# Kernel tuning notes

Measured on AMD Instinct MI355X. Metric: run time of the kernel, lower is better.

The kernel has to match this reference:

```python
import jax, jax.numpy as jnp
import numpy as np

NN = 50000   # num nodes
NE = 10000   # num hyperedges
E = 300000   # num incidences
H = 256      # h_dim == input_dim


def _prelu(x, alpha):
    return jnp.where(x > 0, x, alpha * x)


def setup_inputs() -> dict:
    key = jax.random.key(0)
    ks = jax.random.split(key, 16)
    s = 1.0 / np.sqrt(H)
    inp = {
        "n_feat": jax.random.normal(ks[0], (NN, H), jnp.float32),
        "he_feat": jax.random.normal(ks[1], (NE, H), jnp.float32),
        "node_idx": jax.random.randint(ks[2], (E,), 0, NN),
        "hedge_idx": jax.random.randint(ks[3], (E,), 0, NE),
        # positive degree-style normalization tensors (offset avoids div-by-~0)
        "node_reg_weight": jax.random.uniform(ks[4], (NN,), jnp.float32) + 0.5,
        "node_reg_sum": jax.random.uniform(ks[5], (NN,), jnp.float32) + 0.5,
        "hedge_reg_weight": jax.random.uniform(ks[6], (NE,), jnp.float32) + 0.5,
        "hedge_reg_sum": jax.random.uniform(ks[7], (NE,), jnp.float32) + 0.5,
        # learned params
        "W_in": jax.random.uniform(ks[8], (H, H), jnp.float32, -s, s),
        "b_in": jax.random.uniform(ks[9], (H,), jnp.float32, -s, s),
        "W_n2e": jax.random.uniform(ks[10], (H, H), jnp.float32, -s, s),
        "b_n2e": jax.random.uniform(ks[11], (H,), jnp.float32, -s, s),
        "W_e2n": jax.random.uniform(ks[12], (H, H), jnp.float32, -s, s),
        "b_e2n": jax.random.uniform(ks[13], (H,), jnp.float32, -s, s),
        "alpha": jnp.asarray(0.25, jnp.float32),  # PReLU (single shared param)
    }
    return inp


def reference(n_feat, he_feat, node_idx, hedge_idx,
              node_reg_weight, node_reg_sum, hedge_reg_weight, hedge_reg_sum,
              W_in, b_in, W_n2e, b_n2e, W_e2n, b_e2n, alpha):
    # input2hidden
    nfeat = n_feat @ W_in.T + b_in                       # [NN, H]

    # --- node -> hedge ('in' edges: src=node, dst=hedge) ---
    Wh_n = nfeat @ W_n2e.T + b_n2e                       # [NN, H]
    w_in = node_reg_weight[node_idx] / hedge_reg_sum[hedge_idx]   # [E]
    msg = w_in[:, None] * Wh_n[node_idx]                 # [E, H] gather-multiply
    h_hedge = jax.ops.segment_sum(msg, hedge_idx, num_segments=NE)
    efeat = _prelu(h_hedge, alpha)                       # [NE, H]

    # --- hedge -> node ('con' edges: src=hedge, dst=node) ---
    Wh_e = efeat @ W_e2n.T + b_e2n                       # [NE, H]
    w_con = hedge_reg_weight[hedge_idx] / node_reg_sum[node_idx]  # [E]
    msg2 = w_con[:, None] * Wh_e[hedge_idx]              # [E, H]
    h_node = jax.ops.segment_sum(msg2, node_idx, num_segments=NN)
    nfeat_out = _prelu(h_node, alpha)                    # [NN, H]

    return nfeat_out, efeat
```

## Files before the change

### kernel.cpp

```cpp
#include <hip/hip_runtime.h>

#define NNODE  50000
#define NHEDGE 10000
#define NEDGE  300000
#define HD     256
#define NS     (NHEDGE + NNODE)
#define CVT32_B (((NNODE*HD)/32 + 255) / 256)
#define PAD    32
#define CAP_H  128
#define CAP_N  48

typedef __attribute__((ext_vector_type(8))) short bf16x8;
typedef __attribute__((ext_vector_type(8))) unsigned short u16x8;
typedef __attribute__((ext_vector_type(4))) float f32x4;

__device__ __forceinline__ float prelu(float v, float a){ return v > 0.f ? v : a*v; }
__device__ __forceinline__ unsigned short f2bf(float f){
  unsigned u = __float_as_uint(f);
  return (unsigned short)((u + 0x7FFFu + ((u>>16)&1u)) >> 16);
}
__device__ __forceinline__ float bf2f(unsigned short h){
  return __uint_as_float(((unsigned)h) << 16);
}
__device__ __forceinline__ unsigned f2fp8(float x){
  unsigned u = __float_as_uint(x * 0x1p-120f);
  unsigned s = (u >> 24) & 0x80u;
  unsigned m = u & 0x7fffffffu;
  unsigned r = m + 0x7ffffu + ((m >> 20) & 1u);
  unsigned v = r >> 20;
  if(v > 0x7eu) v = 0x7eu;
  return v | s;
}
__device__ __forceinline__ float fp82f(unsigned b){
  unsigned mag = (b & 0x7fu) << 20;
  float f = __uint_as_float(mag) * 0x1p120f;
  return __uint_as_float(__float_as_uint(f) | ((b & 0x80u) << 24));
}

__global__ __launch_bounds__(256) void k_prep0(
    const float* __restrict__ W_in, const float* __restrict__ b_in,
    const float* __restrict__ W_n2e, const float* __restrict__ b_n2e,
    const float* __restrict__ W_e2n, const float* __restrict__ n_feat,
    const float* __restrict__ nrw,
    unsigned short* __restrict__ Wb0, unsigned short* __restrict__ Wb1,
    float* __restrict__ bc, int* __restrict__ cnts,
    unsigned char* __restrict__ tab8){
  int blk = blockIdx.x, t = threadIdx.x;
  if(blk < HD){
    int o = blk;
    int zi = o*256 + t;
    if(zi < NS) cnts[(size_t)zi*PAD] = 0;
    __shared__ float wn[HD];
    __shared__ float red[4];
    wn[t] = W_n2e[(size_t)o*HD + t];
    __syncthreads();
    float pb = wn[t] * b_in[t];
    #pragma unroll
    for(int d = 32; d > 0; d >>= 1) pb += __shfl_down(pb, d);
    if((t & 63) == 0) red[t >> 6] = pb;
    float acc = 0.f;
    #pragma unroll 8
    for(int h = 0; h < HD; ++h) acc += wn[h] * W_in[(size_t)h*HD + t];
    Wb0[(size_t)o*HD + t] = f2bf(acc);
    Wb1[(size_t)o*HD + t] = f2bf(W_e2n[(size_t)o*HD + t]);
    __syncthreads();
    if(t == 0) bc[o] = red[0] + red[1] + red[2] + red[3] + b_n2e[o];
  } else {
    int t32 = (blk - HD)*256 + t;
    if(t32 >= (NNODE*HD)/32) return;
    size_t f = (size_t)t32 * 32;
    float w = nrw[f >> 8];
    const float4* f4 = (const float4*)(n_feat + f);
    unsigned q[8];
    #pragma unroll
    for(int g = 0; g < 8; ++g){
      float4 a = f4[g];
      q[g] =  f2fp8(w*a.x)        | (f2fp8(w*a.y) << 8)
           | (f2fp8(w*a.z) << 16) | (f2fp8(w*a.w) << 24);
    }
    uint4* out = (uint4*)(tab8 + f);
    out[0] = make_uint4(q[0], q[1], q[2], q[3]);
    out[1] = make_uint4(q[4], q[5], q[6], q[7]);
  }
}

__global__ void k_histfill(const int* __restrict__ node_idx, const int* __restrict__ hedge_idx,
                           const float* __restrict__ nrw, int* __restrict__ cnts,
                           int2* __restrict__ bkt_h, int* __restrict__ bkt_n){
  int e = blockIdx.x*256 + threadIdx.x;
  if(e < NEDGE){
    int j = hedge_idx[e];
    int n = node_idx[e];
    int p = atomicAdd(&cnts[(size_t)j*PAD], 1);
    if(p < CAP_H) bkt_h[(size_t)j*CAP_H + p] = make_int2(n, __float_as_int(nrw[n]));
    int q = atomicAdd(&cnts[(size_t)(NHEDGE + n)*PAD], 1);
    if(q < CAP_N) bkt_n[(size_t)n*CAP_N + q] = j;
  }
}

#define A1_STAGE(V,W) \
    { uint2 cv = V; float cw = W; \
      if(k + 8 < cnt){ int2 s = bh[k+8]; W = __int_as_float(s.y); V = tab[(size_t)s.x*32 + sl]; } \
      acc[0] += fp82f(cv.x);       acc[1] += fp82f(cv.x >> 8); \
      acc[2] += fp82f(cv.x >> 16); acc[3] += fp82f(cv.x >> 24); \
      acc[4] += fp82f(cv.y);       acc[5] += fp82f(cv.y >> 8); \
      acc[6] += fp82f(cv.y >> 16); acc[7] += fp82f(cv.y >> 24); \
      sw += cw; } \
    if(++k >= cnt) break;

__global__ __launch_bounds__(256) void k_agg1(const unsigned char* __restrict__ tab8,
        const int2* __restrict__ bkt_h, const int* __restrict__ cnts,
        unsigned short* __restrict__ aggx_b, float* __restrict__ aggw){
  int wv = threadIdx.x >> 6, lane = threadIdx.x & 63;
  int sub = lane >> 5, sl = lane & 31;
  int j = blockIdx.x*8 + wv*2 + sub;
  int cnt = cnts[(size_t)j*PAD]; if(cnt > CAP_H) cnt = CAP_H;
  const int2* bh = bkt_h + (size_t)j*CAP_H;
  const uint2* tab = (const uint2*)tab8;
  float acc[8] = {0.f,0.f,0.f,0.f,0.f,0.f,0.f,0.f};
  float sw = 0.f;
  uint2 z2 = make_uint2(0,0);
  uint2 v0=z2,v1=z2,v2=z2,v3=z2,v4=z2,v5=z2,v6=z2,v7=z2;
  float w0=0,w1=0,w2=0,w3=0,w4=0,w5=0,w6=0,w7=0;
  if(cnt > 0){ int2 s = bh[0]; w0 = __int_as_float(s.y); v0 = tab[(size_t)s.x*32 + sl]; }
  if(cnt > 1){ int2 s = bh[1]; w1 = __int_as_float(s.y); v1 = tab[(size_t)s.x*32 + sl]; }
  if(cnt > 2){ int2 s = bh[2]; w2 = __int_as_float(s.y); v2 = tab[(size_t)s.x*32 + sl]; }
  if(cnt > 3){ int2 s = bh[3]; w3 = __int_as_float(s.y); v3 = tab[(size_t)s.x*32 + sl]; }
  if(cnt > 4){ int2 s = bh[4]; w4 = __int_as_float(s.y); v4 = tab[(size_t)s.x*32 + sl]; }
  if(cnt > 5){ int2 s = bh[5]; w5 = __int_as_float(s.y); v5 = tab[(size_t)s.x*32 + sl]; }
  if(cnt > 6){ int2 s = bh[6]; w6 = __int_as_float(s.y); v6 = tab[(size_t)s.x*32 + sl]; }
  if(cnt > 7){ int2 s = bh[7]; w7 = __int_as_float(s.y); v7 = tab[(size_t)s.x*32 + sl]; }
  int k = 0;
  while(k < cnt){
    A1_STAGE(v0, w0)
    A1_STAGE(v1, w1)
    A1_STAGE(v2, w2)
    A1_STAGE(v3, w3)
    A1_STAGE(v4, w4)
    A1_STAGE(v5, w5)
    A1_STAGE(v6, w6)
    A1_STAGE(v7, w7)
  }
  u16x8 ob;
  #pragma unroll
  for(int c = 0; c < 8; ++c) ob[c] = f2bf(acc[c]);
  ((u16x8*)aggx_b)[(size_t)j*32 + sl] = ob;
  if(sl == 0) aggw[j] = sw;
}

__global__ __launch_bounds__(256) void k_gemm01(
    const unsigned short* __restrict__ xb, const unsigned short* __restrict__ Wb0,
    const unsigned short* __restrict__ Wb1,
    const float* __restrict__ aggw, const float* __restrict__ hrs,
    const float* __restrict__ hrw, const float* __restrict__ bc,
    const float* __restrict__ be, const float* __restrict__ alpha_p,
    float* __restrict__ out_ef, unsigned short* __restrict__ ef_b,
    unsigned short* __restrict__ y_b){
  int wv = threadIdx.x >> 6, lane = threadIdx.x & 63;
  int m0 = blockIdx.x*32;
  int n0 = wv*64;
  int lr = lane & 15, lk = (lane >> 4) << 3, rb = (lane >> 4) << 2;
  float alpha = *alpha_p;
  const bf16x8 zero8 = {0,0,0,0,0,0,0,0};
  {
    f32x4 acc[2][4];
    #pragma unroll
    for(int a = 0; a < 2; ++a)
      #pragma unroll
      for(int b = 0; b < 4; ++b) acc[a][b] = (f32x4){0.f,0.f,0.f,0.f};
    #pragma unroll
    for(int kc = 0; kc < HD; kc += 32){
      bf16x8 af[2], bfr[4];
      #pragma unroll
      for(int mi = 0; mi < 2; ++mi){
        int r = m0 + mi*16 + lr;
        af[mi] = (r < NHEDGE) ? *(const bf16x8*)&xb[(size_t)r*HD + kc + lk] : zero8;
      }
      #pragma unroll
      for(int ni = 0; ni < 4; ++ni){
        int c = n0 + ni*16 + lr;
        bfr[ni] = *(const bf16x8*)&Wb0[(size_t)c*HD + kc + lk];
      }
      #pragma unroll
      for(int mi = 0; mi < 2; ++mi)
        #pragma unroll
        for(int ni = 0; ni < 4; ++ni)
          acc[mi][ni] = __builtin_amdgcn_mfma_f32_16x16x32_bf16(af[mi], bfr[ni], acc[mi][ni], 0, 0, 0);
    }
    #pragma unroll
    for(int mi = 0; mi < 2; ++mi){
      #pragma unroll
      for(int jj = 0; jj < 4; ++jj){
        int r = m0 + mi*16 + rb + jj;
        if(r < NHEDGE){
          float ra = aggw[r];
          float inv = 1.f / hrs[r];
          #pragma unroll
          for(int ni = 0; ni < 4; ++ni){
            int c = n0 + ni*16 + lr;
            float v = (acc[mi][ni][jj] + ra*bc[c]) * inv;
            v = prelu(v, alpha);
            out_ef[(size_t)r*HD + c] = v;
            ef_b[(size_t)r*HD + c] = f2bf(v);
          }
        }
      }
    }
  }
  __syncthreads();
  {
    f32x4 acc[2][4];
    #pragma unroll
    for(int a = 0; a < 2; ++a)
      #pragma unroll
      for(int b = 0; b < 4; ++b) acc[a][b] = (f32x4){0.f,0.f,0.f,0.f};
    #pragma unroll
    for(int kc = 0; kc < HD; kc += 32){
      bf16x8 af[2], bfr[4];
      #pragma unroll
      for(int mi = 0; mi < 2; ++mi){
        int r = m0 + mi*16 + lr;
        af[mi] = (r < NHEDGE) ? *(const bf16x8*)&ef_b[(size_t)r*HD + kc + lk] : zero8;
      }
      #pragma unroll
      for(int ni = 0; ni < 4; ++ni){
        int c = n0 + ni*16 + lr;
        bfr[ni] = *(const bf16x8*)&Wb1[(size_t)c*HD + kc + lk];
      }
      #pragma unroll
      for(int mi = 0; mi < 2; ++mi)
        #pragma unroll
        for(int ni = 0; ni < 4; ++ni)
          acc[mi][ni] = __builtin_amdgcn_mfma_f32_16x16x32_bf16(af[mi], bfr[ni], acc[mi][ni], 0, 0, 0);
    }
    #pragma unroll
    for(int mi = 0; mi < 2; ++mi){
      #pragma unroll
      for(int jj = 0; jj < 4; ++jj){
        int r = m0 + mi*16 + rb + jj;
        if(r < NHEDGE){
          float ra = hrw[r];
          #pragma unroll
          for(int ni = 0; ni < 4; ++ni){
            int c = n0 + ni*16 + lr;
            float v = ra * (acc[mi][ni][jj] + be[c]);
            y_b[(size_t)r*HD + c] = f2bf(v);
          }
        }
      }
    }
  }
}

__global__ __launch_bounds__(256) void k_agg2(const unsigned short* __restrict__ yb,
        const int* __restrict__ bkt_n, const int* __restrict__ cnts,
        const float* __restrict__ nrs, const float* __restrict__ alpha_p,
        float* __restrict__ out_nodes){
  int wv = threadIdx.x >> 6, lane = threadIdx.x & 63;
  int sub = lane >> 5, sl = lane & 31;
  int i = blockIdx.x*8 + wv*2 + sub;
  int cnt = cnts[(size_t)(NHEDGE + i)*PAD]; if(cnt > CAP_N) cnt = CAP_N;
  const int* bn = bkt_n + (size_t)i*CAP_N;
  const u16x8* tab = (const u16x8*)yb;
  float acc[8] = {0.f,0.f,0.f,0.f,0.f,0.f,0.f,0.f};
  u16x8 z8 = {0,0,0,0,0,0,0,0};
  u16x8 v0=z8, v1=z8, v2=z8, v3=z8;
  if(cnt > 0){ int j = bn[0]; v0 = tab[(size_t)j*32 + sl]; }
  if(cnt > 1){ int j = bn[1]; v1 = tab[(size_t)j*32 + sl]; }
  if(cnt > 2){ int j = bn[2]; v2 = tab[(size_t)j*32 + sl]; }
  if(cnt > 3){ int j = bn[3]; v3 = tab[(size_t)j*32 + sl]; }
  int k = 0;
  while(k < cnt){
    { u16x8 cv = v0;
      if(k + 4 < cnt){ int j = bn[k+4]; v0 = tab[(size_t)j*32 + sl]; }
      #pragma unroll
      for(int c = 0; c < 8; ++c) acc[c] += bf2f(cv[c]); }
    if(++k >= cnt) break;
    { u16x8 cv = v1;
      if(k + 4 < cnt){ int j = bn[k+4]; v1 = tab[(size_t)j*32 + sl]; }
      #pragma unroll
      for(int c = 0; c < 8; ++c) acc[c] += bf2f(cv[c]); }
    if(++k >= cnt) break;
    { u16x8 cv = v2;
      if(k + 4 < cnt){ int j = bn[k+4]; v2 = tab[(size_t)j*32 + sl]; }
      #pragma unroll
      for(int c = 0; c < 8; ++c) acc[c] += bf2f(cv[c]); }
    if(++k >= cnt) break;
    { u16x8 cv = v3;
      if(k + 4 < cnt){ int j = bn[k+4]; v3 = tab[(size_t)j*32 + sl]; }
      #pragma unroll
      for(int c = 0; c < 8; ++c) acc[c] += bf2f(cv[c]); }
    ++k;
  }
  float inv = 1.f / nrs[i];
  float a = *alpha_p;
  float4 o1, o2;
  o1.x = prelu(acc[0]*inv, a); o1.y = prelu(acc[1]*inv, a);
  o1.z = prelu(acc[2]*inv, a); o1.w = prelu(acc[3]*inv, a);
  o2.x = prelu(acc[4]*inv, a); o2.y = prelu(acc[5]*inv, a);
  o2.z = prelu(acc[6]*inv, a); o2.w = prelu(acc[7]*inv, a);
  *(float4*)&out_nodes[(size_t)i*HD + sl*8]     = o1;
  *(float4*)&out_nodes[(size_t)i*HD + sl*8 + 4] = o2;
}

extern "C" void kernel_launch(void* const* d_in, const int* in_sizes, int n_in,
                              void* d_out, int out_size, void* d_ws, size_t ws_size,
                              hipStream_t stream){
  const float* n_feat   = (const float*)d_in[0];
  const int*   node_idx  = (const int*)d_in[2];
  const int*   hedge_idx = (const int*)d_in[3];
  const float* nrw  = (const float*)d_in[4];
  const float* nrs  = (const float*)d_in[5];
  const float* hrw  = (const float*)d_in[6];
  const float* hrs  = (const float*)d_in[7];
  const float* W_in  = (const float*)d_in[8];
  const float* b_in  = (const float*)d_in[9];
  const float* W_n2e = (const float*)d_in[10];
  const float* b_n2e = (const float*)d_in[11];
  const float* W_e2n = (const float*)d_in[12];
  const float* b_e2n = (const float*)d_in[13];
  const float* alpha = (const float*)d_in[14];

  float* out_nodes = (float*)d_out;
  float* out_efeat = out_nodes + (size_t)NNODE * HD;

  unsigned char* tab8 = (unsigned char*)out_nodes;

  char* p = (char*)d_ws;
  auto take = [&](size_t bytes) -> void* {
    void* r = (void*)p;
    p += (bytes + 255) & ~(size_t)255;
    return r;
  };
  unsigned short* Wb0     = (unsigned short*)take((size_t)HD*HD*2);
  unsigned short* Wb1     = (unsigned short*)take((size_t)HD*HD*2);
  float*          bc      = (float*)take(HD*4);
  float*          aggw    = (float*)take(NHEDGE*4);
  unsigned short* aggx_b  = (unsigned short*)take((size_t)NHEDGE*HD*2);
  unsigned short* efeat_b = (unsigned short*)take((size_t)NHEDGE*HD*2);
  int*            cnts    = (int*)take((size_t)NS*PAD*4);
  int2*           bkt_h   = (int2*)take((size_t)NHEDGE*CAP_H*8);
  int*            bkt_n   = (int*)take((size_t)NNODE*CAP_N*4);
  unsigned short* ybuf_b  = aggx_b;

  k_prep0<<<HD + CVT32_B, 256, 0, stream>>>(W_in, b_in, W_n2e, b_n2e, W_e2n,
                                            n_feat, nrw, Wb0, Wb1, bc, cnts, tab8);
  k_histfill<<<(NEDGE+255)/256, 256, 0, stream>>>(node_idx, hedge_idx, nrw,
                                                  cnts, bkt_h, bkt_n);
  k_agg1<<<NHEDGE/8, 256, 0, stream>>>(tab8, bkt_h, cnts, aggx_b, aggw);
  k_gemm01<<<(NHEDGE + 31)/32, 256, 0, stream>>>(aggx_b, Wb0, Wb1, aggw, hrs, hrw,
                                                 bc, b_e2n, alpha,
                                                 out_efeat, efeat_b, ybuf_b);
  k_agg2<<<NNODE/8, 256, 0, stream>>>(ybuf_b, bkt_n, cnts, nrs, alpha, out_nodes);
}
```

Baseline: 150.4 us.

## Split each hyperedge's gather across four half-waves with LDS reduction

k_agg1 now assigns four 32-lane groups to each hyperedge instead of one. Each group takes a quarter of the incidence list, loads its bucket metadata in one coalesced read, broadcasts indices with shuffles, and issues up to 16 independent row gathers before accumulating. The partial sums are then reduced through shared memory. This targets the latency of the serial per-hyperedge gather chain, which averages about 30 incidences, by exposing more parallelism and memory-level concurrency. The cost is four times as many blocks, a __syncthreads, LDS traffic, and more registers for the 16-entry prefetch array.

Result: faster. 133.2 us, median of 2 (-11.4%).

```diff
diff --git a/kernel.cpp b/kernel.cpp
--- a/kernel.cpp
+++ b/kernel.cpp
@@ -98,54 +98,71 @@
   }
 }
 
-#define A1_STAGE(V,W) \
-    { uint2 cv = V; float cw = W; \
-      if(k + 8 < cnt){ int2 s = bh[k+8]; W = __int_as_float(s.y); V = tab[(size_t)s.x*32 + sl]; } \
-      acc[0] += fp82f(cv.x);       acc[1] += fp82f(cv.x >> 8); \
-      acc[2] += fp82f(cv.x >> 16); acc[3] += fp82f(cv.x >> 24); \
-      acc[4] += fp82f(cv.y);       acc[5] += fp82f(cv.y >> 8); \
-      acc[6] += fp82f(cv.y >> 16); acc[7] += fp82f(cv.y >> 24); \
-      sw += cw; } \
-    if(++k >= cnt) break;
-
 __global__ __launch_bounds__(256) void k_agg1(const unsigned char* __restrict__ tab8,
         const int2* __restrict__ bkt_h, const int* __restrict__ cnts,
         unsigned short* __restrict__ aggx_b, float* __restrict__ aggw){
-  int wv = threadIdx.x >> 6, lane = threadIdx.x & 63;
-  int sub = lane >> 5, sl = lane & 31;
-  int j = blockIdx.x*8 + wv*2 + sub;
+  __shared__ float lacc[8][32][9];
+  __shared__ float lsw[8];
+  int tid = threadIdx.x;
+  int half = tid >> 5;
+  int sl   = tid & 31;
+  int lane = tid & 63;
+  int hb   = lane & 32;
+  int j = blockIdx.x*2 + (half >> 2);
+  int c = half & 3;
   int cnt = cnts[(size_t)j*PAD]; if(cnt > CAP_H) cnt = CAP_H;
-  const int2* bh = bkt_h + (size_t)j*CAP_H;
+  int Lc = (cnt + 3) >> 2;
+  int lo = c*Lc; if(lo > cnt) lo = cnt;
+  int hi = lo + Lc; if(hi > cnt) hi = cnt;
+  int Len = hi - lo;
+  const int2* bh = bkt_h + (size_t)j*CAP_H + lo;
+  int2 meta = (sl < Len) ? bh[sl] : make_int2(0, 0);
   const uint2* tab = (const uint2*)tab8;
   float acc[8] = {0.f,0.f,0.f,0.f,0.f,0.f,0.f,0.f};
   float sw = 0.f;
-  uint2 z2 = make_uint2(0,0);
-  uint2 v0=z2,v1=z2,v2=z2,v3=z2,v4=z2,v5=z2,v6=z2,v7=z2;
-  float w0=0,w1=0,w2=0,w3=0,w4=0,w5=0,w6=0,w7=0;
-  if(cnt > 0){ int2 s = bh[0]; w0 = __int_as_float(s.y); v0 = tab[(size_t)s.x*32 + sl]; }
-  if(cnt > 1){ int2 s = bh[1]; w1 = __int_as_float(s.y); v1 = tab[(size_t)s.x*32 + sl]; }
-  if(cnt > 2){ int2 s = bh[2]; w2 = __int_as_float(s.y); v2 = tab[(size_t)s.x*32 + sl]; }
-  if(cnt > 3){ int2 s = bh[3]; w3 = __int_as_float(s.y); v3 = tab[(size_t)s.x*32 + sl]; }
-  if(cnt > 4){ int2 s = bh[4]; w4 = __int_as_float(s.y); v4 = tab[(size_t)s.x*32 + sl]; }
-  if(cnt > 5){ int2 s = bh[5]; w5 = __int_as_float(s.y); v5 = tab[(size_t)s.x*32 + sl]; }
-  if(cnt > 6){ int2 s = bh[6]; w6 = __int_as_float(s.y); v6 = tab[(size_t)s.x*32 + sl]; }
-  if(cnt > 7){ int2 s = bh[7]; w7 = __int_as_float(s.y); v7 = tab[(size_t)s.x*32 + sl]; }
-  int k = 0;
-  while(k < cnt){
-    A1_STAGE(v0, w0)
-    A1_STAGE(v1, w1)
-    A1_STAGE(v2, w2)
-    A1_STAGE(v3, w3)
-    A1_STAGE(v4, w4)
-    A1_STAGE(v5, w5)
-    A1_STAGE(v6, w6)
-    A1_STAGE(v7, w7)
-  }
-  u16x8 ob;
+  uint2 v[16];
   #pragma unroll
-  for(int c = 0; c < 8; ++c) ob[c] = f2bf(acc[c]);
-  ((u16x8*)aggx_b)[(size_t)j*32 + sl] = ob;
-  if(sl == 0) aggw[j] = sw;
+  for(int k = 0; k < 16; ++k){
+    if(k < Len){
+      int src = __shfl(meta.x, hb + k);
+      sw += __int_as_float(__shfl(meta.y, hb + k));
+      v[k] = tab[(size_t)src*32 + sl];
+    }
+  }
+  #pragma unroll
+  for(int k = 0; k < 16; ++k){
+    if(k < Len){
+      uint2 cv = v[k];
+      acc[0] += fp82f(cv.x);       acc[1] += fp82f(cv.x >> 8);
+      acc[2] += fp82f(cv.x >> 16); acc[3] += fp82f(cv.x >> 24);
+      acc[4] += fp82f(cv.y);       acc[5] += fp82f(cv.y >> 8);
+      acc[6] += fp82f(cv.y >> 16); acc[7] += fp82f(cv.y >> 24);
+    }
+  }
+  for(int k = 16; k < Len; ++k){
+    int2 mk = bh[k];
+    sw += __int_as_float(mk.y);
+    uint2 cv = tab[(size_t)mk.x*32 + sl];
+    acc[0] += fp82f(cv.x);       acc[1] += fp82f(cv.x >> 8);
+    acc[2] += fp82f(cv.x >> 16); acc[3] += fp82f(cv.x >> 24);
+    acc[4] += fp82f(cv.y);       acc[5] += fp82f(cv.y >> 8);
+    acc[6] += fp82f(cv.y >> 16); acc[7] += fp82f(cv.y >> 24);
+  }
+  #pragma unroll
+  for(int cc = 0; cc < 8; ++cc) lacc[half][sl][cc] = acc[cc];
+  if(sl == 0) lsw[half] = sw;
+  __syncthreads();
+  if((half & 3) == 0){
+    u16x8 ob;
+    #pragma unroll
+    for(int cc = 0; cc < 8; ++cc){
+      float s = lacc[half][sl][cc] + lacc[half+1][sl][cc]
+              + lacc[half+2][sl][cc] + lacc[half+3][sl][cc];
+      ob[cc] = f2bf(s);
+    }
+    ((u16x8*)aggx_b)[(size_t)j*32 + sl] = ob;
+    if(sl == 0) aggw[j] = lsw[half] + lsw[half+1] + lsw[half+2] + lsw[half+3];
+  }
 }
 
 __global__ __launch_bounds__(256) void k_gemm01(
@@ -347,7 +364,7 @@
                                             n_feat, nrw, Wb0, Wb1, bc, cnts, tab8);
   k_histfill<<<(NEDGE+255)/256, 256, 0, stream>>>(node_idx, hedge_idx, nrw,
                                                   cnts, bkt_h, bkt_n);
-  k_agg1<<<NHEDGE/8, 256, 0, stream>>>(tab8, bkt_h, cnts, aggx_b, aggw);
+  k_agg1<<<NHEDGE/2, 256, 0, stream>>>(tab8, bkt_h, cnts, aggx_b, aggw);
   k_gemm01<<<(NHEDGE + 31)/32, 256, 0, stream>>>(aggx_b, Wb0, Wb1, aggw, hrs, hrw,
                                                  bc, b_e2n, alpha,
                                                  out_efeat, efeat_b, ybuf_b);
```
